# Performance work log

Measured on AMD Instinct MI355X. Metric: run time of the kernel, lower is better.

Reference implementation:

```python
import jax, jax.numpy as jnp
import numpy as np

D_MODEL = 4096
N_EXPERTS = 64
TOP_K = 2


def setup_inputs() -> dict:
    key = jax.random.key(0)
    kx, kw = jax.random.split(key)
    x = jax.random.normal(kx, (4, 8192, D_MODEL), dtype=jnp.float32)
    # nn.Linear(d_model, n_experts, bias=False) weight: [n_experts, d_model]
    W = jax.random.normal(kw, (N_EXPERTS, D_MODEL), dtype=jnp.float32) * (1.0 / np.sqrt(D_MODEL))
    return {"x": x, "W": W}


def reference(x, W):
    # logits: [B, S, n_experts]
    logits = jnp.einsum("bsd,ed->bse", x, W)
    # top-k values and indices along expert dim
    weights, experts = jax.lax.top_k(logits, TOP_K)
    weights = jax.nn.softmax(weights, axis=-1)
    return weights, experts
```

## Files before the change

kernel.cpp:

```cpp
#include <hip/hip_runtime.h>
#include <math.h>

#define D_MODEL 4096
#define N_EXP   64

typedef _Float16 half8 __attribute__((ext_vector_type(8)));
typedef float    f32x4 __attribute__((ext_vector_type(4)));

__global__ __launch_bounds__(256)
void wprep_kernel(const float* __restrict__ W,
                  _Float16* __restrict__ whf, _Float16* __restrict__ wlf) {
    const int gid   = blockIdx.x * 256 + threadIdx.x;
    const int lane  = gid & 63;
    const int ntk   = gid >> 6;
    const int nt    = ntk & 3;
    const int kstep = ntk >> 2;
    const int e  = nt * 16 + (lane & 15);
    const int k0 = kstep * 32 + (lane >> 4) * 8;

    const float* src = W + (size_t)e * D_MODEL + k0;
    float4 w0 = *(const float4*)(src);
    float4 w1 = *(const float4*)(src + 4);
    float wv[8] = {w0.x, w0.y, w0.z, w0.w, w1.x, w1.y, w1.z, w1.w};

    half8 hh, ll;
    #pragma unroll
    for (int j = 0; j < 8; ++j) {
        float ws = wv[j] * 64.0f;
        _Float16 h = (_Float16)ws;
        hh[j] = h;
        ll[j] = (_Float16)((ws - (float)h) * 4096.0f);
    }
    *(half8*)(whf + (size_t)gid * 8) = hh;
    *(half8*)(wlf + (size_t)gid * 8) = ll;
}

#define GLD16(gp, lp) __builtin_amdgcn_global_load_lds( \
    (const __attribute__((address_space(1))) unsigned int*)(const void*)(gp), \
    (__attribute__((address_space(3))) unsigned int*)(void*)(lp), 16, 0, 0)

__device__ __forceinline__ void cvt_hilo(const float4 a, const float4 b,
                                         half8& hi, half8& lo) {
    float av[8] = {a.x, a.y, a.z, a.w, b.x, b.y, b.z, b.w};
    #pragma unroll
    for (int j = 0; j < 8; ++j) {
        _Float16 h = (_Float16)av[j];
        hi[j] = h;
        lo[j] = (_Float16)((av[j] - (float)h) * 4096.0f);
    }
}

__global__ __launch_bounds__(256, 2)
void router_kernel(const float* __restrict__ x,
                   const _Float16* __restrict__ whf,
                   const _Float16* __restrict__ wlf,
                   float* __restrict__ out, int ntok) {
    __shared__ _Float16 sB[2][4][2][4][512];

    const int tid  = threadIdx.x;
    const int w    = tid >> 6;
    const int l    = tid & 63;
    const int tok0 = blockIdx.x * 64;
    const float* ax = x + (size_t)(tok0 + w * 16 + (l & 15)) * D_MODEL + (l >> 4) * 8;

    f32x4 hh[4], cc[4];
    #pragma unroll
    for (int nt = 0; nt < 4; ++nt) { hh[nt] = (f32x4)0.0f; cc[nt] = (f32x4)0.0f; }

    {
        const size_t co = (size_t)w * 4 * 512 + (size_t)l * 8;
        #pragma unroll
        for (int nt = 0; nt < 4; ++nt) {
            GLD16(whf + co + nt * 512, &sB[0][w][0][nt][0]);
            GLD16(wlf + co + nt * 512, &sB[0][w][1][nt][0]);
        }
    }
    float4 P0a = *(const float4*)(ax + 0 * 32), P0b = *(const float4*)(ax + 0 * 32 + 4);
    float4 P1a = *(const float4*)(ax + 1 * 32), P1b = *(const float4*)(ax + 1 * 32 + 4);
    float4 P2a = *(const float4*)(ax + 2 * 32), P2b = *(const float4*)(ax + 2 * 32 + 4);
    float4 P3a = *(const float4*)(ax + 3 * 32), P3b = *(const float4*)(ax + 3 * 32 + 4);
    float4 P4a = *(const float4*)(ax + 4 * 32), P4b = *(const float4*)(ax + 4 * 32 + 4);
    float4 P5a = *(const float4*)(ax + 5 * 32), P5b = *(const float4*)(ax + 5 * 32 + 4);
    float4 P6a = *(const float4*)(ax + 6 * 32), P6b = *(const float4*)(ax + 6 * 32 + 4);
    float4 P7a = *(const float4*)(ax + 7 * 32), P7b = *(const float4*)(ax + 7 * 32 + 4);

    __syncthreads();

#define STEP(KSL, SA, SB, CUR)                                                 \
    {                                                                          \
        half8 ah, al;                                                          \
        cvt_hilo(SA, SB, ah, al);                                              \
        half8 bh[4], bl[4];                                                    \
        _Pragma("unroll")                                                      \
        for (int nt = 0; nt < 4; ++nt) {                                       \
            bh[nt] = *(const half8*)&sB[CUR][KSL][0][nt][l * 8];               \
            bl[nt] = *(const half8*)&sB[CUR][KSL][1][nt][l * 8];               \
        }                                                                      \
        _Pragma("unroll")                                                      \
        for (int nt = 0; nt < 4; ++nt)                                         \
            hh[nt] = __builtin_amdgcn_mfma_f32_16x16x32_f16(ah, bh[nt], hh[nt], 0, 0, 0); \
        _Pragma("unroll")                                                      \
        for (int nt = 0; nt < 4; ++nt)                                         \
            cc[nt] = __builtin_amdgcn_mfma_f32_16x16x32_f16(ah, bl[nt], cc[nt], 0, 0, 0); \
        _Pragma("unroll")                                                      \
        for (int nt = 0; nt < 4; ++nt)                                         \
            cc[nt] = __builtin_amdgcn_mfma_f32_16x16x32_f16(al, bh[nt], cc[nt], 0, 0, 0); \
    }

#define GROUP(G, CUR, C0a,C0b,C1a,C1b,C2a,C2b,C3a,C3b,                         \
                      O0a,O0b,O1a,O1b,O2a,O2b,O3a,O3b)                         \
    {                                                                          \
        if ((G) >= 1 && (G) <= 30) {                                           \
            const size_t kb = (size_t)((G) + 1) * 4 * 32;                      \
            O0a = *(const float4*)(ax + kb + 0 * 32);                          \
            O0b = *(const float4*)(ax + kb + 0 * 32 + 4);                      \
            O1a = *(const float4*)(ax + kb + 1 * 32);                          \
            O1b = *(const float4*)(ax + kb + 1 * 32 + 4);                      \
            O2a = *(const float4*)(ax + kb + 2 * 32);                          \
            O2b = *(const float4*)(ax + kb + 2 * 32 + 4);                      \
            O3a = *(const float4*)(ax + kb + 3 * 32);                          \
            O3b = *(const float4*)(ax + kb + 3 * 32 + 4);                      \
        }                                                                      \
        if ((G) < 31) {                                                        \
            const int ksg = ((G) + 1) * 4 + w;                                 \
            const size_t co = (size_t)ksg * 4 * 512 + (size_t)l * 8;           \
            _Pragma("unroll")                                                  \
            for (int nt = 0; nt < 4; ++nt) {                                   \
                GLD16(whf + co + nt * 512, &sB[(CUR) ^ 1][w][0][nt][0]);       \
                GLD16(wlf + co + nt * 512, &sB[(CUR) ^ 1][w][1][nt][0]);       \
            }                                                                  \
        }                                                                      \
        STEP(0, C0a, C0b, CUR)                                                 \
        STEP(1, C1a, C1b, CUR)                                                 \
        STEP(2, C2a, C2b, CUR)                                                 \
        STEP(3, C3a, C3b, CUR)                                                 \
        __syncthreads();                                                       \
    }

    for (int gg = 0; gg < 16; ++gg) {
        const int g0 = gg * 2;
        GROUP(g0,     0, P0a,P0b,P1a,P1b,P2a,P2b,P3a,P3b,
                         P4a,P4b,P5a,P5b,P6a,P6b,P7a,P7b)
        GROUP(g0 + 1, 1, P4a,P4b,P5a,P5b,P6a,P6b,P7a,P7b,
                         P0a,P0b,P1a,P1b,P2a,P2b,P3a,P3b)
    }
#undef GROUP
#undef STEP

    float tt[4][4];
    #pragma unroll
    for (int nt = 0; nt < 4; ++nt) {
        f32x4 tot = (hh[nt] + cc[nt] * (1.0f / 4096.0f)) * (1.0f / 64.0f);
        tt[nt][0] = tot.x; tt[nt][1] = tot.y; tt[nt][2] = tot.z; tt[nt][3] = tot.w;
    }

    float* out_e = out + (size_t)2 * ntok;

    #pragma unroll
    for (int q = 0; q < 4; ++q) {
        float v1 = -3.0e38f, v2 = -3.0e38f;
        int   i1 = 1 << 30,  i2 = 1 << 30;
        #pragma unroll
        for (int nt = 0; nt < 4; ++nt) {
            float v  = tt[nt][q];
            int   id = nt * 16 + (l & 15);
            if (v > v1 || (v == v1 && id < i1)) {
                v2 = v1; i2 = i1; v1 = v; i1 = id;
            } else if (v > v2 || (v == v2 && id < i2)) {
                v2 = v; i2 = id;
            }
        }
        #pragma unroll
        for (int m = 1; m < 16; m <<= 1) {
            float ov1 = __shfl_xor(v1, m, 64);
            int   oi1 = __shfl_xor(i1, m, 64);
            float ov2 = __shfl_xor(v2, m, 64);
            int   oi2 = __shfl_xor(i2, m, 64);
            bool ofirst = (ov1 > v1) || (ov1 == v1 && oi1 < i1);
            if (ofirst) {
                bool s2 = (ov2 > v1) || (ov2 == v1 && oi2 < i1);
                v2 = s2 ? ov2 : v1;  i2 = s2 ? oi2 : i1;
                v1 = ov1;            i1 = oi1;
            } else {
                bool s2 = (ov1 > v2) || (ov1 == v2 && oi1 < i2);
                v2 = s2 ? ov1 : v2;  i2 = s2 ? oi1 : i2;
            }
        }

        if ((l & 15) == 0) {
            const int tok = tok0 + w * 16 + (l >> 4) * 4 + q;
            float e = expf(v2 - v1);
            float d = 1.0f + e;
            out[2 * tok + 0] = 1.0f / d;
            out[2 * tok + 1] = e / d;
            out_e[2 * tok + 0] = (float)i1;
            out_e[2 * tok + 1] = (float)i2;
        }
    }
}

extern "C" void kernel_launch(void* const* d_in, const int* in_sizes, int n_in,
                              void* d_out, int out_size, void* d_ws, size_t ws_size,
                              hipStream_t stream) {
    const float* x = (const float*)d_in[0];
    const float* W = (const float*)d_in[1];
    float* out = (float*)d_out;
    const int ntok = in_sizes[0] / D_MODEL;

    _Float16* whf = (_Float16*)d_ws;
    _Float16* wlf = (_Float16*)d_ws + (size_t)N_EXP * D_MODEL;

    wprep_kernel<<<dim3(128), dim3(256), 0, stream>>>(W, whf, wlf);
    router_kernel<<<dim3(ntok / 64), dim3(256), 0, stream>>>(x, whf, wlf, out, ntok);
}
```

Before: 129.6 us.

## Stage x tiles through LDS with async global-to-LDS loads instead of register prefetch

Activations are now loaded into a padded LDS buffer with direct global-to-LDS 16-byte loads, double-buffered alongside the W fragments, instead of being prefetched into registers. The k-loop is restructured into 64 stages of 64 elements each, with two MFMA steps per stage and a barrier per stage. This frees the many prefetch registers and makes the x loads more coalesced (row-contiguous per quarter-wave). The cost is twice as many barriers, extra LDS reads of A, and a larger LDS footprint that may limit occupancy.

```diff
diff --git a/kernel.cpp b/kernel.cpp
--- a/kernel.cpp
+++ b/kernel.cpp
@@ -55,41 +55,46 @@
                    const _Float16* __restrict__ whf,
                    const _Float16* __restrict__ wlf,
                    float* __restrict__ out, int ntok) {
-    __shared__ _Float16 sB[2][4][2][4][512];
+    __shared__ __align__(16) float     sA[2 * 4 * 4 * 260];
+    __shared__ __align__(16) _Float16  sB[2][2][2][4][512];
 
     const int tid  = threadIdx.x;
     const int w    = tid >> 6;
     const int l    = tid & 63;
     const int tok0 = blockIdx.x * 64;
-    const float* ax = x + (size_t)(tok0 + w * 16 + (l & 15)) * D_MODEL + (l >> 4) * 8;
+
+    const float* asrc0 = x + (size_t)(tok0 + w * 16 + 0 + (l >> 4)) * D_MODEL + (l & 15) * 4;
+    const float* asrc1 = asrc0 + (size_t)4 * D_MODEL;
+    const float* asrc2 = asrc0 + (size_t)8 * D_MODEL;
+    const float* asrc3 = asrc0 + (size_t)12 * D_MODEL;
+    const _Float16* bsrc = (w >> 1) ? wlf : whf;
 
     f32x4 hh[4], cc[4];
     #pragma unroll
     for (int nt = 0; nt < 4; ++nt) { hh[nt] = (f32x4)0.0f; cc[nt] = (f32x4)0.0f; }
 
-    {
-        const size_t co = (size_t)w * 4 * 512 + (size_t)l * 8;
-        #pragma unroll
-        for (int nt = 0; nt < 4; ++nt) {
-            GLD16(whf + co + nt * 512, &sB[0][w][0][nt][0]);
-            GLD16(wlf + co + nt * 512, &sB[0][w][1][nt][0]);
-        }
+#define STAGE(G, B)                                                            \
+    {                                                                          \
+        const int kf = (G) * 64;                  \
+        GLD16(asrc0 + kf, &sA[(((B) * 4 + w) * 4 + 0) * 260]);                 \
+        GLD16(asrc1 + kf, &sA[(((B) * 4 + w) * 4 + 1) * 260]);                 \
+        GLD16(asrc2 + kf, &sA[(((B) * 4 + w) * 4 + 2) * 260]);                 \
+        GLD16(asrc3 + kf, &sA[(((B) * 4 + w) * 4 + 3) * 260]);                 \
+        const int kst = (G) * 2 + (w & 1);                                     \
+        const size_t bo = (size_t)(kst * 4) * 512 + (size_t)l * 8;             \
+        _Pragma("unroll")                                                      \
+        for (int nt = 0; nt < 4; ++nt)                                         \
+            GLD16(bsrc + bo + nt * 512, &sB[B][w & 1][w >> 1][nt][0]);         \
     }
-    float4 P0a = *(const float4*)(ax + 0 * 32), P0b = *(const float4*)(ax + 0 * 32 + 4);
-    float4 P1a = *(const float4*)(ax + 1 * 32), P1b = *(const float4*)(ax + 1 * 32 + 4);
-    float4 P2a = *(const float4*)(ax + 2 * 32), P2b = *(const float4*)(ax + 2 * 32 + 4);
-    float4 P3a = *(const float4*)(ax + 3 * 32), P3b = *(const float4*)(ax + 3 * 32 + 4);
-    float4 P4a = *(const float4*)(ax + 4 * 32), P4b = *(const float4*)(ax + 4 * 32 + 4);
-    float4 P5a = *(const float4*)(ax + 5 * 32), P5b = *(const float4*)(ax + 5 * 32 + 4);
-    float4 P6a = *(const float4*)(ax + 6 * 32), P6b = *(const float4*)(ax + 6 * 32 + 4);
-    float4 P7a = *(const float4*)(ax + 7 * 32), P7b = *(const float4*)(ax + 7 * 32 + 4);
 
-    __syncthreads();
-
-#define STEP(KSL, SA, SB, CUR)                                                 \
+#define STEP(KSL, CUR)                                                         \
     {                                                                          \
+        const float* ap = &sA[(((CUR) * 4 + w) * 4 + ((l & 15) >> 2)) * 260    \
+                              + ((l & 15) & 3) * 64 + (KSL) * 32 + (l >> 4) * 8]; \
+        float4 a0 = *(const float4*)ap;                                        \
+        float4 a1 = *(const float4*)(ap + 4);                                  \
         half8 ah, al;                                                          \
-        cvt_hilo(SA, SB, ah, al);                                              \
+        cvt_hilo(a0, a1, ah, al);                                              \
         half8 bh[4], bl[4];                                                    \
         _Pragma("unroll")                                                      \
         for (int nt = 0; nt < 4; ++nt) {                                       \
@@ -107,44 +112,21 @@
             cc[nt] = __builtin_amdgcn_mfma_f32_16x16x32_f16(al, bh[nt], cc[nt], 0, 0, 0); \
     }
 
-#define GROUP(G, CUR, C0a,C0b,C1a,C1b,C2a,C2b,C3a,C3b,                         \
-                      O0a,O0b,O1a,O1b,O2a,O2b,O3a,O3b)                         \
-    {                                                                          \
-        if ((G) >= 1 && (G) <= 30) {                                           \
-            const size_t kb = (size_t)((G) + 1) * 4 * 32;                      \
-            O0a = *(const float4*)(ax + kb + 0 * 32);                          \
-            O0b = *(const float4*)(ax + kb + 0 * 32 + 4);                      \
-            O1a = *(const float4*)(ax + kb + 1 * 32);                          \
-            O1b = *(const float4*)(ax + kb + 1 * 32 + 4);                      \
-            O2a = *(const float4*)(ax + kb + 2 * 32);                          \
-            O2b = *(const float4*)(ax + kb + 2 * 32 + 4);                      \
-            O3a = *(const float4*)(ax + kb + 3 * 32);                          \
-            O3b = *(const float4*)(ax + kb + 3 * 32 + 4);                      \
-        }                                                                      \
-        if ((G) < 31) {                                                        \
-            const int ksg = ((G) + 1) * 4 + w;                                 \
-            const size_t co = (size_t)ksg * 4 * 512 + (size_t)l * 8;           \
-            _Pragma("unroll")                                                  \
-            for (int nt = 0; nt < 4; ++nt) {                                   \
-                GLD16(whf + co + nt * 512, &sB[(CUR) ^ 1][w][0][nt][0]);       \
-                GLD16(wlf + co + nt * 512, &sB[(CUR) ^ 1][w][1][nt][0]);       \
-            }                                                                  \
-        }                                                                      \
-        STEP(0, C0a, C0b, CUR)                                                 \
-        STEP(1, C1a, C1b, CUR)                                                 \
-        STEP(2, C2a, C2b, CUR)                                                 \
-        STEP(3, C3a, C3b, CUR)                                                 \
-        __syncthreads();                                                       \
+    STAGE(0, 0)
+    __syncthreads();
+
+    for (int gg = 0; gg < 32; ++gg) {
+        const int g0 = gg * 2;
+        STAGE(g0 + 1, 1)
+        STEP(0, 0)
+        STEP(1, 0)
+        __syncthreads();
+        if (g0 + 2 < 64) STAGE(g0 + 2, 0)
+        STEP(0, 1)
+        STEP(1, 1)
+        __syncthreads();
     }
-
-    for (int gg = 0; gg < 16; ++gg) {
-        const int g0 = gg * 2;
-        GROUP(g0,     0, P0a,P0b,P1a,P1b,P2a,P2b,P3a,P3b,
-                         P4a,P4b,P5a,P5b,P6a,P6b,P7a,P7b)
-        GROUP(g0 + 1, 1, P4a,P4b,P5a,P5b,P6a,P6b,P7a,P7b,
-                         P0a,P0b,P1a,P1b,P2a,P2b,P3a,P3b)
-    }
-#undef GROUP
+#undef STAGE
 #undef STEP
 
     float tt[4][4];
```

After: 152.6 us. 17.7% more time.

## Shrink router blocks to 2 waves and 32 tokens, re-plan LDS staging

Applied to the files above, without the earlier changes.

Each block now handles 32 tokens with 128 threads instead of 64 tokens with 256 threads, so the grid doubles to ntok/32 blocks. The W staging is reorganised so one wave loads the hi halves and the other the lo halves, two k-steps per stage, with the x prefetch ring rotated over four groups instead of two. The aim is more blocks for better load balance and lower per-block LDS. The trade-off is that each block reloads the whole W, doubling total W traffic from L2, and there are twice as many barriers per token of work.

```diff
diff --git a/kernel.cpp b/kernel.cpp
--- a/kernel.cpp
+++ b/kernel.cpp
@@ -50,31 +50,73 @@
     }
 }
 
-__global__ __launch_bounds__(256, 2)
+__global__ __launch_bounds__(128, 2)
 void router_kernel(const float* __restrict__ x,
                    const _Float16* __restrict__ whf,
                    const _Float16* __restrict__ wlf,
                    float* __restrict__ out, int ntok) {
-    __shared__ _Float16 sB[2][4][2][4][512];
+    __shared__ _Float16 sB[2][2][2][4][512];
 
     const int tid  = threadIdx.x;
     const int w    = tid >> 6;
     const int l    = tid & 63;
-    const int tok0 = blockIdx.x * 64;
+    const int tok0 = blockIdx.x * 32;
     const float* ax = x + (size_t)(tok0 + w * 16 + (l & 15)) * D_MODEL + (l >> 4) * 8;
+    const _Float16* bsrc = (w ? wlf : whf) + (size_t)l * 8;
 
     f32x4 hh[4], cc[4];
     #pragma unroll
     for (int nt = 0; nt < 4; ++nt) { hh[nt] = (f32x4)0.0f; cc[nt] = (f32x4)0.0f; }
 
-    {
-        const size_t co = (size_t)w * 4 * 512 + (size_t)l * 8;
-        #pragma unroll
-        for (int nt = 0; nt < 4; ++nt) {
-            GLD16(whf + co + nt * 512, &sB[0][w][0][nt][0]);
-            GLD16(wlf + co + nt * 512, &sB[0][w][1][nt][0]);
-        }
-    }
+#define STAGE(T, BUF)                                                          \
+    {                                                                          \
+        _Pragma("unroll")                                                      \
+        for (int ksl = 0; ksl < 2; ++ksl) {                                    \
+            const int kst = 2 * (T) + ksl;                                     \
+            _Pragma("unroll")                                                  \
+            for (int nt = 0; nt < 4; ++nt)                                     \
+                GLD16(bsrc + (size_t)(kst * 4 + nt) * 512,                     \
+                      &sB[BUF][ksl][w][nt][0]);                                \
+        }                                                                      \
+    }
+
+#define STEP(KSL, SA, SB_, CUR)                                                \
+    {                                                                          \
+        half8 ah, al;                                                          \
+        cvt_hilo(SA, SB_, ah, al);                                             \
+        half8 bh[4], bl[4];                                                    \
+        _Pragma("unroll")                                                      \
+        for (int nt = 0; nt < 4; ++nt) {                                       \
+            bh[nt] = *(const half8*)&sB[CUR][KSL][0][nt][l * 8];               \
+            bl[nt] = *(const half8*)&sB[CUR][KSL][1][nt][l * 8];               \
+        }                                                                      \
+        _Pragma("unroll")                                                      \
+        for (int nt = 0; nt < 4; ++nt)                                         \
+            hh[nt] = __builtin_amdgcn_mfma_f32_16x16x32_f16(ah, bh[nt], hh[nt], 0, 0, 0); \
+        _Pragma("unroll")                                                      \
+        for (int nt = 0; nt < 4; ++nt)                                         \
+            cc[nt] = __builtin_amdgcn_mfma_f32_16x16x32_f16(ah, bl[nt], cc[nt], 0, 0, 0); \
+        _Pragma("unroll")                                                      \
+        for (int nt = 0; nt < 4; ++nt)                                         \
+            cc[nt] = __builtin_amdgcn_mfma_f32_16x16x32_f16(al, bh[nt], cc[nt], 0, 0, 0); \
+    }
+
+#define GROUP(G, CUR, C0a,C0b,C1a,C1b, R0a,R0b,R1a,R1b)                        \
+    {                                                                          \
+        if ((G) >= 1 && (G) <= 60) {                                           \
+            const size_t kb = (size_t)(2 * (G) + 6) * 32;                      \
+            R0a = *(const float4*)(ax + kb);                                   \
+            R0b = *(const float4*)(ax + kb + 4);                               \
+            R1a = *(const float4*)(ax + kb + 32);                              \
+            R1b = *(const float4*)(ax + kb + 36);                              \
+        }                                                                      \
+        if ((G) <= 62) STAGE((G) + 1, (CUR) ^ 1)                               \
+        STEP(0, C0a, C0b, CUR)                                                 \
+        STEP(1, C1a, C1b, CUR)                                                 \
+        __syncthreads();                                                       \
+    }
+
+    STAGE(0, 0)
     float4 P0a = *(const float4*)(ax + 0 * 32), P0b = *(const float4*)(ax + 0 * 32 + 4);
     float4 P1a = *(const float4*)(ax + 1 * 32), P1b = *(const float4*)(ax + 1 * 32 + 4);
     float4 P2a = *(const float4*)(ax + 2 * 32), P2b = *(const float4*)(ax + 2 * 32 + 4);
@@ -83,69 +125,18 @@
     float4 P5a = *(const float4*)(ax + 5 * 32), P5b = *(const float4*)(ax + 5 * 32 + 4);
     float4 P6a = *(const float4*)(ax + 6 * 32), P6b = *(const float4*)(ax + 6 * 32 + 4);
     float4 P7a = *(const float4*)(ax + 7 * 32), P7b = *(const float4*)(ax + 7 * 32 + 4);
-
     __syncthreads();
 
-#define STEP(KSL, SA, SB, CUR)                                                 \
-    {                                                                          \
-        half8 ah, al;                                                          \
-        cvt_hilo(SA, SB, ah, al);                                              \
-        half8 bh[4], bl[4];                                                    \
-        _Pragma("unroll")                                                      \
-        for (int nt = 0; nt < 4; ++nt) {                                       \
-            bh[nt] = *(const half8*)&sB[CUR][KSL][0][nt][l * 8];               \
-            bl[nt] = *(const half8*)&sB[CUR][KSL][1][nt][l * 8];               \
-        }                                                                      \
-        _Pragma("unroll")                                                      \
-        for (int nt = 0; nt < 4; ++nt)                                         \
-            hh[nt] = __builtin_amdgcn_mfma_f32_16x16x32_f16(ah, bh[nt], hh[nt], 0, 0, 0); \
-        _Pragma("unroll")                                                      \
-        for (int nt = 0; nt < 4; ++nt)                                         \
-            cc[nt] = __builtin_amdgcn_mfma_f32_16x16x32_f16(ah, bl[nt], cc[nt], 0, 0, 0); \
-        _Pragma("unroll")                                                      \
-        for (int nt = 0; nt < 4; ++nt)                                         \
-            cc[nt] = __builtin_amdgcn_mfma_f32_16x16x32_f16(al, bh[nt], cc[nt], 0, 0, 0); \
-    }
-
-#define GROUP(G, CUR, C0a,C0b,C1a,C1b,C2a,C2b,C3a,C3b,                         \
-                      O0a,O0b,O1a,O1b,O2a,O2b,O3a,O3b)                         \
-    {                                                                          \
-        if ((G) >= 1 && (G) <= 30) {                                           \
-            const size_t kb = (size_t)((G) + 1) * 4 * 32;                      \
-            O0a = *(const float4*)(ax + kb + 0 * 32);                          \
-            O0b = *(const float4*)(ax + kb + 0 * 32 + 4);                      \
-            O1a = *(const float4*)(ax + kb + 1 * 32);                          \
-            O1b = *(const float4*)(ax + kb + 1 * 32 + 4);                      \
-            O2a = *(const float4*)(ax + kb + 2 * 32);                          \
-            O2b = *(const float4*)(ax + kb + 2 * 32 + 4);                      \
-            O3a = *(const float4*)(ax + kb + 3 * 32);                          \
-            O3b = *(const float4*)(ax + kb + 3 * 32 + 4);                      \
-        }                                                                      \
-        if ((G) < 31) {                                                        \
-            const int ksg = ((G) + 1) * 4 + w;                                 \
-            const size_t co = (size_t)ksg * 4 * 512 + (size_t)l * 8;           \
-            _Pragma("unroll")                                                  \
-            for (int nt = 0; nt < 4; ++nt) {                                   \
-                GLD16(whf + co + nt * 512, &sB[(CUR) ^ 1][w][0][nt][0]);       \
-                GLD16(wlf + co + nt * 512, &sB[(CUR) ^ 1][w][1][nt][0]);       \
-            }                                                                  \
-        }                                                                      \
-        STEP(0, C0a, C0b, CUR)                                                 \
-        STEP(1, C1a, C1b, CUR)                                                 \
-        STEP(2, C2a, C2b, CUR)                                                 \
-        STEP(3, C3a, C3b, CUR)                                                 \
-        __syncthreads();                                                       \
-    }
-
     for (int gg = 0; gg < 16; ++gg) {
-        const int g0 = gg * 2;
-        GROUP(g0,     0, P0a,P0b,P1a,P1b,P2a,P2b,P3a,P3b,
-                         P4a,P4b,P5a,P5b,P6a,P6b,P7a,P7b)
-        GROUP(g0 + 1, 1, P4a,P4b,P5a,P5b,P6a,P6b,P7a,P7b,
-                         P0a,P0b,P1a,P1b,P2a,P2b,P3a,P3b)
+        const int g = gg * 4;
+        GROUP(g + 0, 0, P0a,P0b,P1a,P1b, P6a,P6b,P7a,P7b)
+        GROUP(g + 1, 1, P2a,P2b,P3a,P3b, P0a,P0b,P1a,P1b)
+        GROUP(g + 2, 0, P4a,P4b,P5a,P5b, P2a,P2b,P3a,P3b)
+        GROUP(g + 3, 1, P6a,P6b,P7a,P7b, P4a,P4b,P5a,P5b)
     }
 #undef GROUP
 #undef STEP
+#undef STAGE
 
     float tt[4][4];
     #pragma unroll
@@ -211,5 +202,5 @@
     _Float16* wlf = (_Float16*)d_ws + (size_t)N_EXP * D_MODEL;
 
     wprep_kernel<<<dim3(128), dim3(256), 0, stream>>>(W, whf, wlf);
-    router_kernel<<<dim3(ntok / 64), dim3(256), 0, stream>>>(x, whf, wlf, out, ntok);
-}
+    router_kernel<<<dim3(ntok / 32), dim3(128), 0, stream>>>(x, whf, wlf, out, ntok);
+}
```

Measured after the change: 157.5 us. +21.5%, slower.
